# Performance work log

Hardware: AMD Instinct MI355X
Metric: run time of the kernel (lower is better)

Reference implementation:

```python
import jax, jax.numpy as jnp
import numpy as np

B = 1024        # batch_size (len(c_ids))
D = 128         # dim_proto
N_AFE_A = 2     # len(AFE_a_ids_selected) == l_a
N_AFE_R = 2     # len(AFE_r_ids_selected) == l_r
S = 16          # sum(n_nbs_per_hop) = 10 + 6
A = 4096        # num_atoms (active codebook rows)
L = N_AFE_A + N_AFE_R * S  # 34


def _normalize(x, eps=1e-12):
    # torch F.normalize(dim=-1): x / max(||x||_2, eps)
    n = jnp.linalg.norm(x, axis=-1, keepdims=True)
    return x / jnp.maximum(n, eps)


def setup_inputs() -> dict:
    key = jax.random.key(0)
    k1, k2, k3 = jax.random.split(key, 3)
    embeddings = jax.random.normal(k1, (B, L, D), dtype=jnp.float32)
    atoms = jax.random.uniform(k2, (A, D), dtype=jnp.float32, minval=0.0, maxval=0.5)
    W_att = jax.random.normal(k3, ((N_AFE_A + N_AFE_R * S) * D, N_AFE_R * S + N_AFE_A), dtype=jnp.float32) * 0.02
    b_att = jnp.zeros((N_AFE_R * S + N_AFE_A,), dtype=jnp.float32)
    return {"embeddings": embeddings, "atoms": atoms, "W_att": W_att, "b_att": b_att}


def reference(embeddings, atoms, W_att, b_att):
    atoms_n = _normalize(atoms)  # F.normalize(self.atoms[0:num_atoms], dim=-1), [A, D]

    # --- attribute emb sets: embeddings[:, i, :] for i in range(n_AFE_a) ---
    attr = embeddings[:, :N_AFE_A, :]                                 # [B, la, D]
    soft_a = jnp.einsum('bld,ad->bla', attr, atoms_n)                 # similarity vs codebook
    hard_a = (soft_a == soft_a.max(axis=-1, keepdims=True)).astype(jnp.float32)
    assoc_a = jnp.einsum('bla,ad->bld', hard_a, atoms)                # one-hot @ atoms (lookup)

    # --- relational emb sets: chunks of size S, flattened to [B*S, D] in torch ---
    rel = embeddings[:, N_AFE_A:, :].reshape(B, N_AFE_R, S, D)
    soft_r = jnp.einsum('brsd,ad->brsa', rel, atoms_n)
    hard_r = (soft_r == soft_r.max(axis=-1, keepdims=True)).astype(jnp.float32)
    assoc_r = jnp.einsum('brsa,ad->brsd', hard_r, atoms).reshape(B, N_AFE_R * S, D)

    # per-row L2 normalize each associated prototype, then concat along slot dim
    assoc = jnp.concatenate([_normalize(assoc_a), _normalize(assoc_r)], axis=1)  # [B, la+lr*S, D]

    # attention aggregation: Linear over flattened slots, then bmm
    a = assoc.reshape(B, (N_AFE_A + N_AFE_R * S) * D)
    att = a @ W_att + b_att                                           # [B, la+lr*S]
    obj_embs = _normalize(jnp.einsum('bl,bld->bd', att, assoc))       # [B, D]
    return obj_embs
```

## Files before the change

kernel.cpp:

```cpp
#include <hip/hip_runtime.h>
#include <math.h>

#define BB 1024
#define LL 34
#define DD 128
#define AA 4096
#define NROWS (BB * LL)
#define RTILES (NROWS / 16)
#define ATILES (AA / 16)
#define NSPLIT 8
#define TPS (ATILES / NSPLIT)
#define NCHUNK (TPS / 4)
#define TAU 2.5e-3f

typedef _Float16 f16;
typedef _Float16 f16x8 __attribute__((ext_vector_type(8)));
typedef float f32x4  __attribute__((ext_vector_type(4)));

#define OFF_EMBA   0u
#define OFF_ATOMB  8912896u
#define OFF_WFRAG  9961472u
#define OFF_G      10379264u
#define OFF_PQ     30433280u
#define OFF_INVN64 34889728u
#define OFF_INVNF  34922496u

__global__ __launch_bounds__(256) void k_prep(const float* __restrict__ emb,
                                              const float* __restrict__ atoms,
                                              const float* __restrict__ W,
                                              double* __restrict__ invn64,
                                              float* __restrict__ invnF,
                                              f16x8* __restrict__ embA,
                                              f16x8* __restrict__ atomB,
                                              f16x8* __restrict__ wfrag) {
    __shared__ double part[16][17];
    const int bid = blockIdx.x;
    const int tid = threadIdx.x;

    if (bid < RTILES) {
        const int ks = tid >> 6, l = tid & 63;
        const int m = l & 15, koff = ((l >> 4) << 3) + (ks << 5);
        const float* p = emb + (size_t)(bid * 16 + m) * DD + koff;
        float4 f0 = ((const float4*)p)[0];
        float4 f1 = ((const float4*)p)[1];
        float xs[8] = {f0.x, f0.y, f0.z, f0.w, f1.x, f1.y, f1.z, f1.w};
        f16x8 h;
        #pragma unroll
        for (int j = 0; j < 8; j++) h[j] = (f16)xs[j];
        embA[(size_t)(bid * 4 + ks) * 64 + l] = h;
    } else if (bid < RTILES + ATILES) {
        const int tile = bid - RTILES;
        const int ks = tid >> 6, l = tid & 63;
        const int m = l & 15, koff = ((l >> 4) << 3) + (ks << 5);
        const float* p = atoms + (size_t)(tile * 16 + m) * DD + koff;
        float4 f0 = ((const float4*)p)[0];
        float4 f1 = ((const float4*)p)[1];
        float xs[8] = {f0.x, f0.y, f0.z, f0.w, f1.x, f1.y, f1.z, f1.w};
        double ssq = 0.0;
        #pragma unroll
        for (int j = 0; j < 8; j++) ssq += (double)xs[j] * xs[j];
        part[m][ks * 4 + (l >> 4)] = ssq;
        __syncthreads();
        double tot = 0.0;
        #pragma unroll
        for (int q = 0; q < 16; q++) tot += part[m][q];
        double n = sqrt(tot);
        if (n < 1e-12) n = 1e-12;
        double inv = 1.0 / n;
        float invf = (float)inv;
        f16x8 h;
        #pragma unroll
        for (int j = 0; j < 8; j++) h[j] = (f16)(xs[j] * invf);
        if (ks == 0 && (l >> 4) == 0) {
            invn64[tile * 16 + m] = inv;
            invnF[tile * 16 + m] = invf;
        }
        atomB[(size_t)(tile * 4 + ks) * 64 + l] = h;
    } else {
        const int l = bid - RTILES - ATILES;
        for (int s = tid; s < 768; s += 256) {
            int lane = s & 63, ksnt = s >> 6;
            int ks = ksnt & 3, nt = ksnt >> 2;
            int j = nt * 16 + (lane & 15);
            int kb = ks * 32 + ((lane >> 4) << 3);
            f16x8 h;
            if (j < LL) {
                const float* wp = W + (size_t)(l * 128 + kb) * LL + j;
                #pragma unroll
                for (int jj = 0; jj < 8; jj++) h[jj] = (f16)wp[jj * LL];
            } else {
                #pragma unroll
                for (int jj = 0; jj < 8; jj++) h[jj] = (f16)0.f;
            }
            wfrag[(size_t)((l * 3 + nt) * 4 + ks) * 64 + lane] = h;
        }
    }
}

__global__ __launch_bounds__(256) void k_gtab(const f16x8* __restrict__ atomB,
                                              const f16x8* __restrict__ wfrag,
                                              float* __restrict__ G) {
    const int bid = blockIdx.x;
    const int l = bid >> 4, ag = bid & 15;
    const int w = threadIdx.x >> 6, lane = threadIdx.x & 63;

    f16x8 bw[3][4];
    #pragma unroll
    for (int nt = 0; nt < 3; nt++)
        #pragma unroll
        for (int ks = 0; ks < 4; ks++)
            bw[nt][ks] = wfrag[(size_t)((l * 3 + nt) * 4 + ks) * 64 + lane];

    const int col = lane & 15, rq = (lane >> 4) * 4;
    #pragma unroll
    for (int t = 0; t < 4; t++) {
        int atile = ag * 16 + w * 4 + t;
        f16x8 ah[4];
        #pragma unroll
        for (int ks = 0; ks < 4; ks++)
            ah[ks] = atomB[(size_t)(atile * 4 + ks) * 64 + lane];
        f32x4 acc[3];
        #pragma unroll
        for (int nt = 0; nt < 3; nt++) acc[nt] = (f32x4){0.f, 0.f, 0.f, 0.f};
        #pragma unroll
        for (int ks = 0; ks < 4; ks++)
            #pragma unroll
            for (int nt = 0; nt < 3; nt++)
                acc[nt] = __builtin_amdgcn_mfma_f32_16x16x32_f16(ah[ks], bw[nt][ks], acc[nt], 0, 0, 0);
        int a0 = atile * 16 + rq;
        #pragma unroll
        for (int nt = 0; nt < 3; nt++) {
            int j = nt * 16 + col;
            if (j < LL) {
                #pragma unroll
                for (int r = 0; r < 4; r++)
                    G[((size_t)(a0 + r) * LL + l) * 36 + j] = acc[nt][r];
            }
        }
    }
}

__global__ __launch_bounds__(256, 3) void k_score(const f16x8* __restrict__ embA,
                                                  const char* __restrict__ atomB,
                                                  float4* __restrict__ pq) {
    __shared__ __align__(16) char sbuf[2][16384];

    const int tid = threadIdx.x;
    const int w = tid >> 6, l = tid & 63;
    const int rb = blockIdx.x >> 3, sp = blockIdx.x & 7;
    const int rt0 = rb * 16 + w * 4;

    f16x8 a[4][4];
    #pragma unroll
    for (int f = 0; f < 4; f++)
        #pragma unroll
        for (int ks = 0; ks < 4; ks++)
            a[f][ks] = embA[(size_t)((rt0 + f) * 4 + ks) * 64 + l];

    float v1[16], v2[16];
    #pragma unroll
    for (int s = 0; s < 16; s++) { v1[s] = -3e38f; v2[s] = -3e38f; }

    #define STAGE(C, BUF)                                                          \
        {                                                                          \
            size_t _tb = (size_t)(sp * TPS + (C) * 4) * 4096;                      \
            _Pragma("unroll")                                                      \
            for (int r = 0; r < 4; r++) {                                          \
                const char* _src = atomB + _tb + r * 4096;                         \
                uint32_t* _dst = (uint32_t*)(&sbuf[BUF][0] + r * 4096 + w * 1024); \
                __builtin_amdgcn_global_load_lds((const uint32_t*)(_src + tid * 16), \
                                                 _dst, 16, 0, 0);                  \
            }                                                                      \
        }

    STAGE(0, 0);
    __syncthreads();

    for (int c = 0; c < NCHUNK; c++) {
        const int buf = c & 1;
        if (c + 1 < NCHUNK) STAGE(c + 1, buf ^ 1);

        #pragma unroll
        for (int tt = 0; tt < 4; tt++) {
            f16x8 bh[4];
            #pragma unroll
            for (int ks = 0; ks < 4; ks++)
                bh[ks] = *(const f16x8*)(&sbuf[buf][0] + tt * 4096 + ks * 1024 + l * 16);
            f32x4 acc[4];
            #pragma unroll
            for (int f = 0; f < 4; f++) acc[f] = (f32x4){0.f, 0.f, 0.f, 0.f};
            #pragma unroll
            for (int ks = 0; ks < 4; ks++)
                #pragma unroll
                for (int f = 0; f < 4; f++)
                    acc[f] = __builtin_amdgcn_mfma_f32_16x16x32_f16(a[f][ks], bh[ks], acc[f], 0, 0, 0);
            const unsigned tl = (unsigned)(c * 4 + tt);
            #pragma unroll
            for (int f = 0; f < 4; f++)
                #pragma unroll
                for (int r = 0; r < 4; r++) {
                    int s = f * 4 + r;
                    float xq = __uint_as_float((__float_as_uint(acc[f][r]) & 0xFFFFFFE0u) | tl);
                    v2[s] = __builtin_amdgcn_fmed3f(xq, v1[s], v2[s]);
                    v1[s] = fmaxf(v1[s], xq);
                }
        }
        __syncthreads();
    }
    #undef STAGE

    float vv1[16], vv2[16];
    int jj1[16], jj2[16];
    const int col = l & 15;
    #pragma unroll
    for (int s = 0; s < 16; s++) {
        unsigned u1 = __float_as_uint(v1[s]);
        unsigned u2 = __float_as_uint(v2[s]);
        vv1[s] = __uint_as_float(u1 & 0xFFFFFFE0u);
        vv2[s] = __uint_as_float(u2 & 0xFFFFFFE0u);
        jj1[s] = (sp * TPS + (int)(u1 & 31u)) * 16 + col;
        jj2[s] = (sp * TPS + (int)(u2 & 31u)) * 16 + col;
    }

    #pragma unroll
    for (int m = 1; m <= 8; m <<= 1) {
        #pragma unroll
        for (int s = 0; s < 16; s++) {
            float ov1 = __shfl_xor(vv1[s], m);
            float ov2 = __shfl_xor(vv2[s], m);
            int   oi1 = __shfl_xor(jj1[s], m);
            int   oi2 = __shfl_xor(jj2[s], m);
            bool sel = ov1 > vv1[s];
            float lv  = sel ? vv1[s] : ov1;
            int   li  = sel ? jj1[s] : oi1;
            float wv2 = sel ? ov2 : vv2[s];
            int   wi2 = sel ? oi2 : jj2[s];
            vv1[s] = sel ? ov1 : vv1[s];
            jj1[s] = sel ? oi1 : jj1[s];
            bool s2 = lv > wv2;
            vv2[s] = s2 ? lv : wv2;
            jj2[s] = s2 ? li : wi2;
        }
    }

    if ((l & 15) == 0) {
        int q = l >> 4;
        #pragma unroll
        for (int f = 0; f < 4; f++)
            #pragma unroll
            for (int r = 0; r < 4; r++) {
                int s = f * 4 + r;
                int row = (rt0 + f) * 16 + q * 4 + r;
                float4 o;
                o.x = vv1[s];
                o.y = vv2[s];
                o.z = __int_as_float(jj1[s]);
                o.w = __int_as_float(jj2[s]);
                pq[(size_t)row * NSPLIT + sp] = o;
            }
    }
}

__global__ __launch_bounds__(256) void k_epilogue(const float4* __restrict__ pq,
                                                  const float* __restrict__ emb,
                                                  const float* __restrict__ atoms,
                                                  const double* __restrict__ invn64,
                                                  const float* __restrict__ invnF,
                                                  const float* __restrict__ G,
                                                  const float* __restrict__ b_att,
                                                  float* __restrict__ out) {
    __shared__ __align__(16) float assoc[LL * DD];
    __shared__ int   amaxS[LL];
    __shared__ float invS[LL];
    __shared__ float attS[LL];
    __shared__ float wsum[4][40];
    __shared__ float sqw[4];
    __shared__ int   flagCnt;
    __shared__ int   flagRow[LL];

    const int b = blockIdx.x, tid = threadIdx.x;
    const int wid = tid >> 6, lane = tid & 63;

    if (tid == 0) flagCnt = 0;
    __syncthreads();

    if (tid < LL) {
        size_t base = (size_t)(b * LL + tid) * NSPLIT;
        float V1 = -3e38f, V2 = -3e38f;
        int I1 = 0;
        #pragma unroll
        for (int sp = 0; sp < NSPLIT; sp++) {
            float4 qv = pq[base + sp];
            float a1 = qv.x, a2 = qv.y;
            int   j1 = __float_as_int(qv.z);
            bool sel = a1 > V1;
            float lv  = sel ? V1 : a1;
            float wv2 = sel ? a2 : V2;
            V1 = sel ? a1 : V1;
            I1 = sel ? j1 : I1;
            V2 = fmaxf(lv, wv2);
        }
        amaxS[tid] = I1;
        if (V1 - V2 < TAU) {
            int k = atomicAdd(&flagCnt, 1);
            flagRow[k] = tid;
        }
    }
    __syncthreads();

    const int cnt = flagCnt;
    for (int fi = wid; fi < cnt; fi += 4) {
        int row = flagRow[fi];
        const float2 ev = ((const float2*)(emb + (size_t)(b * LL + row) * DD))[lane];
        size_t base = (size_t)(b * LL + row) * NSPLIT;
        double bestS = -1e300;
        int bestI = 0x7fffffff;
        for (int sp = 0; sp < NSPLIT; sp++) {
            float4 qv = pq[base + sp];
            #pragma unroll
            for (int h = 0; h < 2; h++) {
                int idx = __float_as_int(h ? qv.w : qv.z);
                const float2 av = ((const float2*)(atoms + (size_t)idx * DD))[lane];
                double p = (double)ev.x * av.x + (double)ev.y * av.y;
                #pragma unroll
                for (int m = 1; m <= 32; m <<= 1) p += __shfl_xor(p, m);
                double sc = p * invn64[idx];
                if (sc > bestS || (sc == bestS && idx < bestI)) { bestS = sc; bestI = idx; }
            }
        }
        if (lane == 0) amaxS[row] = bestI;
    }
    __syncthreads();

    if (tid < LL) invS[tid] = invnF[amaxS[tid]];
    if (lane < LL) {
        float ga = 0.f;
        for (int ll = wid; ll < LL; ll += 4)
            ga += G[((size_t)amaxS[ll] * LL + ll) * 36 + lane];
        wsum[wid][lane] = ga;
    }
    __syncthreads();

    for (int idx = tid; idx < LL * DD; idx += 256) {
        int ll = idx >> 7, d = idx & 127;
        assoc[idx] = atoms[(size_t)amaxS[ll] * DD + d] * invS[ll];
    }
    if (tid < LL)
        attS[tid] = b_att[tid] + wsum[0][tid] + wsum[1][tid] + wsum[2][tid] + wsum[3][tid];
    __syncthreads();

    float o = 0.0f;
    if (tid < DD) {
        #pragma unroll
        for (int ll = 0; ll < LL; ll++) o = fmaf(attS[ll], assoc[ll * DD + tid], o);
    }
    float sq = (tid < DD) ? o * o : 0.0f;
    #pragma unroll
    for (int off = 32; off; off >>= 1) sq += __shfl_xor(sq, off);
    if (lane == 0) sqw[wid] = sq;
    __syncthreads();
    float tot = sqw[0] + sqw[1] + sqw[2] + sqw[3];
    float n = sqrtf(tot);
    float inv = 1.0f / fmaxf(n, 1e-12f);
    if (tid < DD) out[(size_t)b * DD + tid] = o * inv;
}

extern "C" void kernel_launch(void* const* d_in, const int* in_sizes, int n_in,
                              void* d_out, int out_size, void* d_ws, size_t ws_size,
                              hipStream_t stream) {
    const float* emb   = (const float*)d_in[0];
    const float* atoms = (const float*)d_in[1];
    const float* W     = (const float*)d_in[2];
    const float* b_att = (const float*)d_in[3];
    float* out = (float*)d_out;

    char* ws = (char*)d_ws;
    f16x8*  embA   = (f16x8*)(ws + OFF_EMBA);
    char*   atomB  = (char*)(ws + OFF_ATOMB);
    f16x8*  wfrag  = (f16x8*)(ws + OFF_WFRAG);
    float*  G      = (float*)(ws + OFF_G);
    float4* pq     = (float4*)(ws + OFF_PQ);
    double* invn64 = (double*)(ws + OFF_INVN64);
    float*  invnF  = (float*)(ws + OFF_INVNF);

    k_prep<<<RTILES + ATILES + LL, 256, 0, stream>>>(emb, atoms, W, invn64, invnF,
                                                     embA, (f16x8*)atomB, wfrag);
    k_gtab<<<LL * 16, 256, 0, stream>>>((const f16x8*)atomB, wfrag, G);
    k_score<<<(RTILES / 16) * NSPLIT, 256, 0, stream>>>(embA, atomB, pq);
    k_epilogue<<<BB, 256, 0, stream>>>(pq, emb, atoms, invn64, invnF, G, b_att, out);
}
```

Baseline: 166.5 us.

## Merge G-table kernel into score launch and stage prep loads through LDS

Removes the separate k_gtab launch by appending its blocks to the k_score grid, so the G table is built alongside scoring. G blocks write results to LDS first and then store them coalesced, using a new layout indexed by slot then atom. k_prep now reads embedding, atom and W tiles into padded shared memory with coalesced loads before building the fragments. The epilogue caches its pq rows in LDS, and the score block order is remapped so blocks with the same split index sit next to each other. The cost is extra shared-memory use and branchy mixed-role blocks in the score kernel.

```diff
diff --git a/kernel.cpp b/kernel.cpp
--- a/kernel.cpp
+++ b/kernel.cpp
@@ -12,6 +12,8 @@
 #define TPS (ATILES / NSPLIT)
 #define NCHUNK (TPS / 4)
 #define TAU 2.5e-3f
+#define SCOREBLKS ((RTILES / 16) * NSPLIT)
+#define GTABBLKS (LL * 32)
 
 typedef _Float16 f16;
 typedef _Float16 f16x8 __attribute__((ext_vector_type(8)));
@@ -33,51 +35,63 @@
                                               f16x8* __restrict__ embA,
                                               f16x8* __restrict__ atomB,
                                               f16x8* __restrict__ wfrag) {
+    __shared__ __align__(16) float stbuf[4608];
     __shared__ double part[16][17];
     const int bid = blockIdx.x;
     const int tid = threadIdx.x;
 
-    if (bid < RTILES) {
+    if (bid < RTILES + ATILES) {
+        const bool isAtom = (bid >= RTILES);
+        const int tile = isAtom ? bid - RTILES : bid;
+        const float* src = (isAtom ? atoms : emb) + (size_t)tile * 2048;
+        float4* st4 = (float4*)stbuf;
+        for (int i = tid; i < 512; i += 256) {
+            int row = i >> 5, c4 = i & 31;
+            st4[row * 33 + c4] = ((const float4*)src)[i];
+        }
+        __syncthreads();
+
         const int ks = tid >> 6, l = tid & 63;
-        const int m = l & 15, koff = ((l >> 4) << 3) + (ks << 5);
-        const float* p = emb + (size_t)(bid * 16 + m) * DD + koff;
-        float4 f0 = ((const float4*)p)[0];
-        float4 f1 = ((const float4*)p)[1];
+        const int m = l & 15, koff4 = ((l >> 4) << 1) + (ks << 3);
+        float4 f0 = st4[m * 33 + koff4];
+        float4 f1 = st4[m * 33 + koff4 + 1];
         float xs[8] = {f0.x, f0.y, f0.z, f0.w, f1.x, f1.y, f1.z, f1.w};
-        f16x8 h;
-        #pragma unroll
-        for (int j = 0; j < 8; j++) h[j] = (f16)xs[j];
-        embA[(size_t)(bid * 4 + ks) * 64 + l] = h;
-    } else if (bid < RTILES + ATILES) {
-        const int tile = bid - RTILES;
-        const int ks = tid >> 6, l = tid & 63;
-        const int m = l & 15, koff = ((l >> 4) << 3) + (ks << 5);
-        const float* p = atoms + (size_t)(tile * 16 + m) * DD + koff;
-        float4 f0 = ((const float4*)p)[0];
-        float4 f1 = ((const float4*)p)[1];
-        float xs[8] = {f0.x, f0.y, f0.z, f0.w, f1.x, f1.y, f1.z, f1.w};
-        double ssq = 0.0;
-        #pragma unroll
-        for (int j = 0; j < 8; j++) ssq += (double)xs[j] * xs[j];
-        part[m][ks * 4 + (l >> 4)] = ssq;
-        __syncthreads();
-        double tot = 0.0;
-        #pragma unroll
-        for (int q = 0; q < 16; q++) tot += part[m][q];
-        double n = sqrt(tot);
-        if (n < 1e-12) n = 1e-12;
-        double inv = 1.0 / n;
-        float invf = (float)inv;
-        f16x8 h;
-        #pragma unroll
-        for (int j = 0; j < 8; j++) h[j] = (f16)(xs[j] * invf);
-        if (ks == 0 && (l >> 4) == 0) {
-            invn64[tile * 16 + m] = inv;
-            invnF[tile * 16 + m] = invf;
-        }
-        atomB[(size_t)(tile * 4 + ks) * 64 + l] = h;
+
+        if (!isAtom) {
+            f16x8 h;
+            #pragma unroll
+            for (int j = 0; j < 8; j++) h[j] = (f16)xs[j];
+            embA[(size_t)(tile * 4 + ks) * 64 + l] = h;
+        } else {
+            double ssq = 0.0;
+            #pragma unroll
+            for (int j = 0; j < 8; j++) ssq += (double)xs[j] * xs[j];
+            part[m][ks * 4 + (l >> 4)] = ssq;
+            __syncthreads();
+            double tot = 0.0;
+            #pragma unroll
+            for (int q = 0; q < 16; q++) tot += part[m][q];
+            double n = sqrt(tot);
+            if (n < 1e-12) n = 1e-12;
+            double inv = 1.0 / n;
+            float invf = (float)inv;
+            f16x8 h;
+            #pragma unroll
+            for (int j = 0; j < 8; j++) h[j] = (f16)(xs[j] * invf);
+            if (ks == 0 && (l >> 4) == 0) {
+                invn64[tile * 16 + m] = inv;
+                invnF[tile * 16 + m] = invf;
+            }
+            atomB[(size_t)(tile * 4 + ks) * 64 + l] = h;
+        }
     } else {
         const int l = bid - RTILES - ATILES;
+        const float* wsrc = W + (size_t)l * 128 * LL;
+        for (int i = tid; i < 128 * LL; i += 256) {
+            int row = i / LL, j = i - row * LL;
+            stbuf[row * 35 + j] = wsrc[i];
+        }
+        __syncthreads();
         for (int s = tid; s < 768; s += 256) {
             int lane = s & 63, ksnt = s >> 6;
             int ks = ksnt & 3, nt = ksnt >> 2;
@@ -85,9 +99,8 @@
             int kb = ks * 32 + ((lane >> 4) << 3);
             f16x8 h;
             if (j < LL) {
-                const float* wp = W + (size_t)(l * 128 + kb) * LL + j;
-                #pragma unroll
-                for (int jj = 0; jj < 8; jj++) h[jj] = (f16)wp[jj * LL];
+                #pragma unroll
+                for (int jj = 0; jj < 8; jj++) h[jj] = (f16)stbuf[(kb + jj) * 35 + j];
             } else {
                 #pragma unroll
                 for (int jj = 0; jj < 8; jj++) h[jj] = (f16)0.f;
@@ -97,57 +110,62 @@
     }
 }
 
-__global__ __launch_bounds__(256) void k_gtab(const f16x8* __restrict__ atomB,
-                                              const f16x8* __restrict__ wfrag,
-                                              float* __restrict__ G) {
-    const int bid = blockIdx.x;
-    const int l = bid >> 4, ag = bid & 15;
-    const int w = threadIdx.x >> 6, lane = threadIdx.x & 63;
-
-    f16x8 bw[3][4];
-    #pragma unroll
-    for (int nt = 0; nt < 3; nt++)
-        #pragma unroll
-        for (int ks = 0; ks < 4; ks++)
-            bw[nt][ks] = wfrag[(size_t)((l * 3 + nt) * 4 + ks) * 64 + lane];
-
-    const int col = lane & 15, rq = (lane >> 4) * 4;
-    #pragma unroll
-    for (int t = 0; t < 4; t++) {
-        int atile = ag * 16 + w * 4 + t;
-        f16x8 ah[4];
-        #pragma unroll
-        for (int ks = 0; ks < 4; ks++)
-            ah[ks] = atomB[(size_t)(atile * 4 + ks) * 64 + lane];
-        f32x4 acc[3];
-        #pragma unroll
-        for (int nt = 0; nt < 3; nt++) acc[nt] = (f32x4){0.f, 0.f, 0.f, 0.f};
-        #pragma unroll
-        for (int ks = 0; ks < 4; ks++)
-            #pragma unroll
-            for (int nt = 0; nt < 3; nt++)
-                acc[nt] = __builtin_amdgcn_mfma_f32_16x16x32_f16(ah[ks], bw[nt][ks], acc[nt], 0, 0, 0);
-        int a0 = atile * 16 + rq;
-        #pragma unroll
-        for (int nt = 0; nt < 3; nt++) {
-            int j = nt * 16 + col;
-            if (j < LL) {
-                #pragma unroll
-                for (int r = 0; r < 4; r++)
-                    G[((size_t)(a0 + r) * LL + l) * 36 + j] = acc[nt][r];
-            }
-        }
-    }
-}
-
 __global__ __launch_bounds__(256, 3) void k_score(const f16x8* __restrict__ embA,
                                                   const char* __restrict__ atomB,
+                                                  const f16x8* __restrict__ wfrag,
+                                                  float* __restrict__ G,
                                                   float4* __restrict__ pq) {
-    __shared__ __align__(16) char sbuf[2][16384];
-
+    __shared__ __align__(16) char shmem[32768];
     const int tid = threadIdx.x;
     const int w = tid >> 6, l = tid & 63;
-    const int rb = blockIdx.x >> 3, sp = blockIdx.x & 7;
+
+    if (blockIdx.x >= SCOREBLKS) {
+        const int gb = blockIdx.x - SCOREBLKS;
+        const int ll = gb >> 5, ab = gb & 31;
+        float* gs = (float*)shmem;
+
+        f16x8 bw[3][4];
+        #pragma unroll
+        for (int nt = 0; nt < 3; nt++)
+            #pragma unroll
+            for (int ks = 0; ks < 4; ks++)
+                bw[nt][ks] = wfrag[(size_t)((ll * 3 + nt) * 4 + ks) * 64 + l];
+
+        const int col = l & 15, rq = (l >> 4) * 4;
+        #pragma unroll
+        for (int t = 0; t < 2; t++) {
+            int atile = ab * 8 + w * 2 + t;
+            f16x8 ah[4];
+            #pragma unroll
+            for (int ks = 0; ks < 4; ks++)
+                ah[ks] = *(const f16x8*)(atomB + ((size_t)(atile * 4 + ks) * 64 + l) * 16);
+            f32x4 acc[3];
+            #pragma unroll
+            for (int nt = 0; nt < 3; nt++) acc[nt] = (f32x4){0.f, 0.f, 0.f, 0.f};
+            #pragma unroll
+            for (int ks = 0; ks < 4; ks++)
+                #pragma unroll
+                for (int nt = 0; nt < 3; nt++)
+                    acc[nt] = __builtin_amdgcn_mfma_f32_16x16x32_f16(ah[ks], bw[nt][ks], acc[nt], 0, 0, 0);
+            int aloc0 = (w * 2 + t) * 16 + rq;
+            #pragma unroll
+            for (int nt = 0; nt < 3; nt++) {
+                int j = nt * 16 + col;
+                if (j < LL) {
+                    #pragma unroll
+                    for (int r = 0; r < 4; r++)
+                        gs[(aloc0 + r) * 36 + j] = acc[nt][r];
+                }
+            }
+        }
+        __syncthreads();
+        float* Gl = G + ((size_t)ll * 4096 + ab * 128) * 36;
+        for (int i = tid; i < 128 * 36; i += 256) Gl[i] = gs[i];
+        return;
+    }
+
+    char (*sbuf)[16384] = (char(*)[16384])shmem;
+    const int sp = blockIdx.x / 136, rb = blockIdx.x - sp * 136;
     const int rt0 = rb * 16 + w * 4;
 
     f16x8 a[4][4];
@@ -270,6 +288,7 @@
                                                   const float* __restrict__ b_att,
                                                   float* __restrict__ out) {
     __shared__ __align__(16) float assoc[LL * DD];
+    __shared__ __align__(16) float4 pqS[LL][NSPLIT];
     __shared__ int   amaxS[LL];
     __shared__ float invS[LL];
     __shared__ float attS[LL];
@@ -282,15 +301,16 @@
     const int wid = tid >> 6, lane = tid & 63;
 
     if (tid == 0) flagCnt = 0;
+    for (int i = tid; i < LL * NSPLIT; i += 256)
+        pqS[i >> 3][i & 7] = pq[(size_t)(b * LL + (i >> 3)) * NSPLIT + (i & 7)];
     __syncthreads();
 
     if (tid < LL) {
-        size_t base = (size_t)(b * LL + tid) * NSPLIT;
         float V1 = -3e38f, V2 = -3e38f;
         int I1 = 0;
         #pragma unroll
         for (int sp = 0; sp < NSPLIT; sp++) {
-            float4 qv = pq[base + sp];
+            float4 qv = pqS[tid][sp];
             float a1 = qv.x, a2 = qv.y;
             int   j1 = __float_as_int(qv.z);
             bool sel = a1 > V1;
@@ -312,11 +332,10 @@
     for (int fi = wid; fi < cnt; fi += 4) {
         int row = flagRow[fi];
         const float2 ev = ((const float2*)(emb + (size_t)(b * LL + row) * DD))[lane];
-        size_t base = (size_t)(b * LL + row) * NSPLIT;
         double bestS = -1e300;
         int bestI = 0x7fffffff;
         for (int sp = 0; sp < NSPLIT; sp++) {
-            float4 qv = pq[base + sp];
+            float4 qv = pqS[row][sp];
             #pragma unroll
             for (int h = 0; h < 2; h++) {
                 int idx = __float_as_int(h ? qv.w : qv.z);
@@ -336,7 +355,7 @@
     if (lane < LL) {
         float ga = 0.f;
         for (int ll = wid; ll < LL; ll += 4)
-            ga += G[((size_t)amaxS[ll] * LL + ll) * 36 + lane];
+            ga += G[((size_t)ll * 4096 + amaxS[ll]) * 36 + lane];
         wsum[wid][lane] = ga;
     }
     __syncthreads();
@@ -385,7 +404,6 @@
 
     k_prep<<<RTILES + ATILES + LL, 256, 0, stream>>>(emb, atoms, W, invn64, invnF,
                                                      embA, (f16x8*)atomB, wfrag);
-    k_gtab<<<LL * 16, 256, 0, stream>>>((const f16x8*)atomB, wfrag, G);
-    k_score<<<(RTILES / 16) * NSPLIT, 256, 0, stream>>>(embA, atomB, pq);
+    k_score<<<SCOREBLKS + GTABBLKS, 256, 0, stream>>>(embA, atomB, wfrag, G, pq);
     k_epilogue<<<BB, 256, 0, stream>>>(pq, emb, atoms, invn64, invnF, G, b_att, out);
 }
```

After: 157.6 us. 5.3% less time.
